# Kernel tuning notes

Measured on AMD Instinct MI355X. Metric: run time of the kernel, lower is better.

The kernel has to match this reference:

```python
import jax, jax.numpy as jnp
import numpy as np

T_KD = 20.0      # KL_divergence temperature
T_THR = 6.0      # Threshold_weights temperature
EPS = 1e-05


def _margin(o, gathered):
    # torch.sort descending, take top-2; margin only when target is the argmax value
    top2 = jax.lax.top_k(o, 2)[0]                      # [B, 2]
    return jnp.where(top2[:, 0] == gathered, top2[:, 0] - top2[:, 1], 0.0)


def _forward(outputs1, outputs2, outputs3, outputs4, out_s, targets):
    B = targets.shape[0]
    idx = jnp.arange(B)
    mimic = (outputs1 + outputs2 + outputs3 + outputs4) / 4.0

    teachers = [outputs1, outputs2, outputs3, outputs4, mimic]
    gathered = [t[idx, targets] for t in teachers]      # each [B]

    # C = min over gathered target logits of the 4 real teachers
    C = jnp.minimum(jnp.minimum(gathered[0].min(), gathered[1].min()),
                    jnp.minimum(gathered[2].min(), gathered[3].min()))
    # if C < 0: shift everything by (-C + eps); else no shift
    shift = jnp.where(C < 0, -C + EPS, 0.0)

    shifted = [t + shift for t in teachers]
    g_shift = [g + shift for g in gathered]

    # Threshold_weights: margin per branch, softmax over 5 branches
    preds = jnp.stack([_margin(s, g) for s, g in zip(shifted, g_shift)], axis=1)  # [B,5]
    out_threshold = jax.nn.softmax(preds / T_THR, axis=1)

    # max over the 4 (shifted) teacher logit tensors
    max_preds = jnp.maximum(jnp.maximum(shifted[0].max(), shifted[1].max()),
                            jnp.maximum(shifted[2].max(), shifted[3].max()))

    # per-sample CE of student (shared across branches)
    log_p_s = jax.nn.log_softmax(out_s, axis=1)
    CE = -log_p_s[idx, targets]                          # [B]

    log_ps_T = jax.nn.log_softmax(out_s / T_KD, axis=1)  # [B,C]

    def branch_loss(teacher, g_s):
        w2 = g_s / max_preds          # weights2
        w1 = 1.0 - w2                 # weights1
        log_pt = jax.nn.log_softmax(teacher / T_KD, axis=1)
        p_t = jnp.exp(log_pt)
        KD = jnp.sum(p_t * (log_pt - log_ps_T), axis=1) * (T_KD * T_KD)  # [B]
        return w1 * CE + w2 * KD

    # KD/CE use the ORIGINAL (unshifted) teacher logits
    losses = jnp.stack([branch_loss(t, g) for t, g in zip(teachers, g_shift)], axis=1)  # [B,5]
    return jnp.mean(jnp.sum(out_threshold * losses, axis=1))


def setup_inputs() -> dict:
    key = jax.random.key(0)
    ks = jax.random.split(key, 6)
    B, C = 8192, 1000
    return {
        "outputs1": jax.random.normal(ks[0], (B, C), dtype=jnp.float32),
        "outputs2": jax.random.normal(ks[1], (B, C), dtype=jnp.float32),
        "outputs3": jax.random.normal(ks[2], (B, C), dtype=jnp.float32),
        "outputs4": jax.random.normal(ks[3], (B, C), dtype=jnp.float32),
        "out_s": jax.random.normal(ks[4], (B, C), dtype=jnp.float32),
        "targets": jax.random.randint(ks[5], (B,), 0, C, dtype=jnp.int64 if jax.config.jax_enable_x64 else jnp.int32),
    }


def reference(outputs1, outputs2, outputs3, outputs4, out_s, targets):
    return _forward(outputs1, outputs2, outputs3, outputs4, out_s, targets)
```

## Files before the change

kernel.cpp:

```cpp
#include <hip/hip_runtime.h>
#include <math.h>

#define NB 8192
#define NC 1000
#define NF4 250


#define LOG2E 1.4426950408889634f
#define LN2   0.6931471805599453f
#define K20C  (LOG2E / 20.0f)

__device__ __forceinline__ float fexp2(float x) { return __builtin_amdgcn_exp2f(x); }
__device__ __forceinline__ float flog2(float x) { return __builtin_amdgcn_logf(x); }

#define VMWAIT0                                          \
  asm volatile("s_waitcnt vmcnt(0)" ::: "memory");       \
  __builtin_amdgcn_sched_barrier(0)
#define LGKM0                                            \
  asm volatile("s_waitcnt lgkmcnt(0)" ::: "memory");     \
  __builtin_amdgcn_sched_barrier(0)

typedef const __attribute__((address_space(1))) unsigned int gu32;
typedef __attribute__((address_space(3))) unsigned int lu32;
__device__ __forceinline__ void stage16(const void* g, void* l) {
  __builtin_amdgcn_global_load_lds((gu32*)g, (lu32*)l, 16, 0, 0);
}

template <int CTRL>
__device__ __forceinline__ float dpp_mov(float v, float ident) {
  return __uint_as_float((unsigned)__builtin_amdgcn_update_dpp(
      (int)__float_as_uint(ident), (int)__float_as_uint(v), CTRL, 0xF, 0xF,
      false));
}

__device__ __forceinline__ float dppredsum(float v) {
  v += dpp_mov<0x111>(v, 0.f);
  v += dpp_mov<0x112>(v, 0.f);
  v += dpp_mov<0x114>(v, 0.f);
  v += dpp_mov<0x118>(v, 0.f);
  v += dpp_mov<0x142>(v, 0.f);
  v += dpp_mov<0x143>(v, 0.f);
  return v;
}

__device__ __forceinline__ void dppredtop2(float& t1, float& t2) {
  const float NI = -INFINITY;
#define T2STEP(C)                                   \
  {                                                 \
    float i1 = dpp_mov<C>(t1, NI);                  \
    float i2 = dpp_mov<C>(t2, NI);                  \
    t2 = fmaxf(fmaxf(t2, i2), fminf(t1, i1));       \
    t1 = fmaxf(t1, i1);                             \
  }
  T2STEP(0x111) T2STEP(0x112) T2STEP(0x114) T2STEP(0x118)
  T2STEP(0x142) T2STEP(0x143)
#undef T2STEP
}

__device__ __forceinline__ float wredsum(float v) {
#pragma unroll
  for (int m = 32; m >= 1; m >>= 1) v += __shfl_xor(v, m, 64);
  return v;
}
__device__ __forceinline__ float wredmax(float v) {
#pragma unroll
  for (int m = 32; m >= 1; m >>= 1) v = fmaxf(v, __shfl_xor(v, m, 64));
  return v;
}
__device__ __forceinline__ float wredmin(float v) {
#pragma unroll
  for (int m = 32; m >= 1; m >>= 1) v = fminf(v, __shfl_xor(v, m, 64));
  return v;
}
__device__ __forceinline__ float f4get(const float4& v, int e) {
  return e == 0 ? v.x : e == 1 ? v.y : e == 2 ? v.z : v.w;
}
__device__ __forceinline__ float& f4ref(float4& v, int e) {
  return e == 0 ? v.x : e == 1 ? v.y : e == 2 ? v.z : v.w;
}

__device__ __forceinline__ void proc_mat(const float4& c, const float4& cs,
                                         float& t1, float& t2, float& Zm,
                                         float& S1m, float4& sum4) {
#pragma unroll
  for (int e = 0; e < 4; ++e) {
    float w = f4get(c, e);
    float wsv = f4get(cs, e);
    t2 = fmaxf(t2, fminf(t1, w));
    t1 = fmaxf(t1, w);
    float et = fexp2(w * K20C);
    Zm += et;
    S1m = fmaf(et, w - wsv, S1m);
    f4ref(sum4, e) += w;
  }
}

__global__ __launch_bounds__(256, 4) void k_rowstats(
    const float* __restrict__ o1, const float* __restrict__ o2,
    const float* __restrict__ o3, const float* __restrict__ o4,
    const float* __restrict__ os, const int* __restrict__ tg,
    float* __restrict__ ws, float* __restrict__ out) {
  const int lane = threadIdx.x & 63;
  const int wv = threadIdx.x >> 6;
  const int row = (blockIdx.x << 2) + wv;
  const size_t base = (size_t)row * NC;

  __shared__ float4 lds[4][5][64];

  if (blockIdx.x == 0 && threadIdx.x == 0) out[0] = 0.0f;

  const int target = tg[row];

#define STAGE(i)                                                          \
  do {                                                                    \
    int f_ = lane + ((i) << 6);                                           \
    if (f_ > NF4 - 1) f_ = NF4 - 1;    \
    stage16((const float4*)(o1 + base) + f_, &lds[wv][0][0]);             \
    stage16((const float4*)(o2 + base) + f_, &lds[wv][1][0]);             \
    stage16((const float4*)(o3 + base) + f_, &lds[wv][2][0]);             \
    stage16((const float4*)(o4 + base) + f_, &lds[wv][3][0]);             \
    stage16((const float4*)(os + base) + f_, &lds[wv][4][0]);             \
  } while (0)

  STAGE(0);

  float t1[5], t2[5], Z[5], S1[5];
#pragma unroll
  for (int t = 0; t < 5; ++t) {
    t1[t] = -INFINITY; t2[t] = -INFINITY; Z[t] = 0.f; S1[t] = 0.f;
  }
  float Z1 = 0.f, Z20 = 0.f;

#define CHUNK(ACT, STAGE_STMT)                                            \
  do {                                                                    \
    VMWAIT0;                                                              \
    float4 rs_ = lds[wv][4][lane];                                        \
    float4 sum4_ = {0.f, 0.f, 0.f, 0.f};                                  \
    float4 cm_;                                                           \
    cm_ = lds[wv][0][lane];                                               \
    if (ACT) proc_mat(cm_, rs_, t1[0], t2[0], Z[0], S1[0], sum4_);        \
    cm_ = lds[wv][1][lane];                                               \
    if (ACT) proc_mat(cm_, rs_, t1[1], t2[1], Z[1], S1[1], sum4_);        \
    cm_ = lds[wv][2][lane];                                               \
    if (ACT) proc_mat(cm_, rs_, t1[2], t2[2], Z[2], S1[2], sum4_);        \
    cm_ = lds[wv][3][lane];                                               \
    if (ACT) proc_mat(cm_, rs_, t1[3], t2[3], Z[3], S1[3], sum4_);        \
    LGKM0;     \
    STAGE_STMT;                                                           \
    if (ACT) {                                                            \
      _Pragma("unroll")                                                   \
      for (int e = 0; e < 4; ++e) {                                       \
        float wsv = f4get(rs_, e);                                        \
        float wm = f4get(sum4_, e) * 0.25f;                    \
        t2[4] = fmaxf(t2[4], fminf(t1[4], wm));                           \
        t1[4] = fmaxf(t1[4], wm);                                         \
        float et = fexp2(wm * K20C);                                      \
        Z[4] += et;                                                       \
        S1[4] = fmaf(et, wm - wsv, S1[4]);                                \
        Z1 += fexp2(wsv * LOG2E);                                         \
        Z20 += fexp2(wsv * K20C);                                         \
      }                                                                   \
    }                                                                     \
  } while (0)

  CHUNK(true, STAGE(1));
  CHUNK(true, STAGE(2));
  CHUNK(true, STAGE(3));
  CHUNK(lane < 58, );

  const float g1 = o1[base + target];
  const float g2 = o2[base + target];
  const float g3 = o3[base + target];
  const float g4 = o4[base + target];
  const float gs = os[base + target];

#pragma unroll
  for (int t = 0; t < 5; ++t) dppredtop2(t1[t], t2[t]);
#pragma unroll
  for (int t = 0; t < 5; ++t) { Z[t] = dppredsum(Z[t]); S1[t] = dppredsum(S1[t]); }
  Z1 = dppredsum(Z1);
  Z20 = dppredsum(Z20);

  if (lane == 63) {
    const float gm = ((g1 + g2) + g3 + g4) * 0.25f;
    float gg[5] = {g1, g2, g3, g4, gm};

    const float lse_s = flog2(Z20) * LN2;
    const float CE = flog2(Z1) * LN2 - gs;

#pragma unroll
    for (int t = 0; t < 5; ++t) {
      float lse_t = flog2(Z[t]) * LN2;
      float KD = 400.0f * (S1[t] / (20.0f * Z[t]) - lse_t + lse_s);
      float margin = (t1[t] == gg[t]) ? (t1[t] - t2[t]) : 0.0f;
      ws[(size_t)t * NB + row] = margin;
      ws[(size_t)(5 + t) * NB + row] = gg[t];
      ws[(size_t)(10 + t) * NB + row] = KD;
    }
    ws[(size_t)15 * NB + row] = CE;
    ws[(size_t)16 * NB + row] = fminf(fminf(g1, g2), fminf(g3, g4));
    ws[(size_t)17 * NB + row] = fmaxf(fmaxf(t1[0], t1[1]), fmaxf(t1[2], t1[3]));
  }
#undef STAGE
#undef CHUNK
}

__global__ __launch_bounds__(64) void k_final(const float* __restrict__ ws,
                                              float* __restrict__ out) {
  const int lane = threadIdx.x;

  float mn = INFINITY, mx = -INFINITY;
  const float4* mnp = (const float4*)(ws + (size_t)16 * NB);
  const float4* mxp = (const float4*)(ws + (size_t)17 * NB);
#pragma unroll
  for (int k = 0; k < 32; ++k) {
    int r4 = lane + (k << 6);
    float4 a = mnp[r4];
    float4 b = mxp[r4];
    mn = fminf(mn, fminf(fminf(a.x, a.y), fminf(a.z, a.w)));
    mx = fmaxf(mx, fmaxf(fmaxf(b.x, b.y), fmaxf(b.z, b.w)));
  }
  mn = wredmin(mn);
  mx = wredmax(mx);
  const float shift = (mn < 0.0f) ? (-mn + 1e-5f) : 0.0f;
  const float maxp = mx + shift;

  const int r = blockIdx.x * 64 + lane;
  const float K6 = LOG2E / 6.0f;

  float m[5], e[5];
#pragma unroll
  for (int t = 0; t < 5; ++t) m[t] = ws[(size_t)t * NB + r];
  float pm = fmaxf(fmaxf(fmaxf(m[0], m[1]), fmaxf(m[2], m[3])), m[4]);
  float Zl = 0.0f;
#pragma unroll
  for (int t = 0; t < 5; ++t) { e[t] = fexp2((m[t] - pm) * K6); Zl += e[t]; }
  float ce = ws[(size_t)15 * NB + r];
  float rl = 0.0f;
#pragma unroll
  for (int t = 0; t < 5; ++t) {
    float g = ws[(size_t)(5 + t) * NB + r];
    float kd = ws[(size_t)(10 + t) * NB + r];
    float w2 = (g + shift) / maxp;
    float loss = (1.0f - w2) * ce + w2 * kd;
    rl += e[t] * loss;
  }
  float acc = wredsum(rl / Zl);
  if (lane == 0) atomicAdd(out, acc * (1.0f / 8192.0f));
}

extern "C" void kernel_launch(void* const* d_in, const int* in_sizes, int n_in,
                              void* d_out, int out_size, void* d_ws, size_t ws_size,
                              hipStream_t stream) {
  const float* o1 = (const float*)d_in[0];
  const float* o2 = (const float*)d_in[1];
  const float* o3 = (const float*)d_in[2];
  const float* o4 = (const float*)d_in[3];
  const float* os = (const float*)d_in[4];
  const int* tg = (const int*)d_in[5];
  float* ws = (float*)d_ws;
  float* out = (float*)d_out;

  k_rowstats<<<NB / 4, 256, 0, stream>>>(o1, o2, o3, o4, os, tg, ws, out);
  k_final<<<NB / 64, 64, 0, stream>>>(ws, out);
}
```

Measured before the change: 187.4 us.

## Double-buffer LDS staging across four rows per wave with partial vmcnt waits

Each wave now processes four rows instead of one, using a two-slot LDS ring so the next chunk's global-to-LDS loads are in flight while the current chunk is computed. Partial s_waitcnt vmcnt counts replace full drains, and the target-logit gathers are issued early and overlapped with the streaming loads. The grid shrinks by four. The goal is to hide memory latency in this bandwidth-bound pass, at the cost of fewer blocks and fragile hand-counted wait values.

Result: no change. 189.9 us (+1.3%).

```diff
diff --git a/kernel.cpp b/kernel.cpp
--- a/kernel.cpp
+++ b/kernel.cpp
@@ -13,9 +13,10 @@
 __device__ __forceinline__ float fexp2(float x) { return __builtin_amdgcn_exp2f(x); }
 __device__ __forceinline__ float flog2(float x) { return __builtin_amdgcn_logf(x); }
 
-#define VMWAIT0                                          \
-  asm volatile("s_waitcnt vmcnt(0)" ::: "memory");       \
+#define VMWAIT_(N)                                       \
+  asm volatile("s_waitcnt vmcnt(" #N ")" ::: "memory");  \
   __builtin_amdgcn_sched_barrier(0)
+#define VMWAIT(N) VMWAIT_(N)
 #define LGKM0                                            \
   asm volatile("s_waitcnt lgkmcnt(0)" ::: "memory");     \
   __builtin_amdgcn_sched_barrier(0)
@@ -102,56 +103,98 @@
     float* __restrict__ ws, float* __restrict__ out) {
   const int lane = threadIdx.x & 63;
   const int wv = threadIdx.x >> 6;
-  const int row = (blockIdx.x << 2) + wv;
-  const size_t base = (size_t)row * NC;
-
-  __shared__ float4 lds[4][5][64];
+  const int rowbase = (blockIdx.x * 4 + wv) * 4;
+  __shared__ float4 lds[4][2][5][64];
 
   if (blockIdx.x == 0 && threadIdx.x == 0) out[0] = 0.0f;
 
-  const int target = tg[row];
-
-#define STAGE(i)                                                          \
-  do {                                                                    \
-    int f_ = lane + ((i) << 6);                                           \
+  int tgv = tg[rowbase + (lane & 3)];
+
+#define STAGES(s)                                                         \
+  do {                                                                    \
+    const int r_ = (s) >> 2, c_ = (s) & 3;                                \
+    const size_t b_ = (size_t)(rowbase + r_) * NC;                        \
+    int f_ = lane + (c_ << 6);                                            \
     if (f_ > NF4 - 1) f_ = NF4 - 1;    \
-    stage16((const float4*)(o1 + base) + f_, &lds[wv][0][0]);             \
-    stage16((const float4*)(o2 + base) + f_, &lds[wv][1][0]);             \
-    stage16((const float4*)(o3 + base) + f_, &lds[wv][2][0]);             \
-    stage16((const float4*)(o4 + base) + f_, &lds[wv][3][0]);             \
-    stage16((const float4*)(os + base) + f_, &lds[wv][4][0]);             \
-  } while (0)
-
-  STAGE(0);
-
-  float t1[5], t2[5], Z[5], S1[5];
-#pragma unroll
-  for (int t = 0; t < 5; ++t) {
-    t1[t] = -INFINITY; t2[t] = -INFINITY; Z[t] = 0.f; S1[t] = 0.f;
-  }
-  float Z1 = 0.f, Z20 = 0.f;
-
-#define CHUNK(ACT, STAGE_STMT)                                            \
-  do {                                                                    \
-    VMWAIT0;                                                              \
-    float4 rs_ = lds[wv][4][lane];                                        \
+    stage16((const float4*)(o1 + b_) + f_, &lds[wv][(s) & 1][0][0]);      \
+    stage16((const float4*)(o2 + b_) + f_, &lds[wv][(s) & 1][1][0]);      \
+    stage16((const float4*)(o3 + b_) + f_, &lds[wv][(s) & 1][2][0]);      \
+    stage16((const float4*)(o4 + b_) + f_, &lds[wv][(s) & 1][3][0]);      \
+    stage16((const float4*)(os + b_) + f_, &lds[wv][(s) & 1][4][0]);      \
+  } while (0)
+
+#define GATHER(r)                                                         \
+  do {                                                                    \
+    const int tgt_ = __shfl(tgv, (r), 64);                                \
+    const size_t gb_ = (size_t)(rowbase + (r)) * NC + tgt_;               \
+    g1 = o1[gb_]; g2 = o2[gb_]; g3 = o3[gb_]; g4 = o4[gb_]; g5 = os[gb_]; \
+  } while (0)
+
+  STAGES(0);
+  STAGES(1);
+
+  float t1[5], t2[5], Z[5], S1[5], Z1, Z20;
+  float g1, g2, g3, g4, g5;
+#define RESETACC                                                          \
+  do {                                                                    \
+    _Pragma("unroll") for (int t = 0; t < 5; ++t) {                       \
+      t1[t] = -INFINITY; t2[t] = -INFINITY; Z[t] = 0.f; S1[t] = 0.f;      \
+    }                                                                     \
+    Z1 = 0.f; Z20 = 0.f;                                                  \
+  } while (0)
+  RESETACC;
+
+#define REDUCE_EPI(r)                                                     \
+  do {                                                                    \
+    _Pragma("unroll") for (int t = 0; t < 5; ++t) dppredtop2(t1[t], t2[t]); \
+    _Pragma("unroll") for (int t = 0; t < 5; ++t) {                       \
+      Z[t] = dppredsum(Z[t]); S1[t] = dppredsum(S1[t]);                   \
+    }                                                                     \
+    Z1 = dppredsum(Z1);                                                   \
+    Z20 = dppredsum(Z20);                                                 \
+    if (lane == 63) {                                                     \
+      const int row_ = rowbase + (r);                                     \
+      const float gm_ = ((g1 + g2) + g3 + g4) * 0.25f;                    \
+      float gg_[5] = {g1, g2, g3, g4, gm_};                               \
+      const float lse_s_ = flog2(Z20) * LN2;                              \
+      const float CE_ = flog2(Z1) * LN2 - g5;                             \
+      _Pragma("unroll") for (int t = 0; t < 5; ++t) {                     \
+        float lse_t_ = flog2(Z[t]) * LN2;                                 \
+        float KD_ = 400.0f * (S1[t] / (20.0f * Z[t]) - lse_t_ + lse_s_);  \
+        float mg_ = (t1[t] == gg_[t]) ? (t1[t] - t2[t]) : 0.0f;           \
+        ws[(size_t)t * NB + row_] = mg_;                                  \
+        ws[(size_t)(5 + t) * NB + row_] = gg_[t];                         \
+        ws[(size_t)(10 + t) * NB + row_] = KD_;                           \
+      }                                                                   \
+      ws[(size_t)15 * NB + row_] = CE_;                                   \
+      ws[(size_t)16 * NB + row_] = fminf(fminf(g1, g2), fminf(g3, g4));   \
+      ws[(size_t)17 * NB + row_] =                                        \
+          fmaxf(fmaxf(t1[0], t1[1]), fmaxf(t1[2], t1[3]));                \
+    }                                                                     \
+    RESETACC;                                                             \
+  } while (0)
+
+#define SLOT(WAITN, BUF, ACT, STAGE_STMT, GATHER_STMT, ROWEND_STMT)       \
+  do {                                                                    \
+    VMWAIT(WAITN);                                                        \
+    float4 rs_ = lds[wv][BUF][4][lane];                                   \
     float4 sum4_ = {0.f, 0.f, 0.f, 0.f};                                  \
     float4 cm_;                                                           \
-    cm_ = lds[wv][0][lane];                                               \
+    cm_ = lds[wv][BUF][0][lane];                                          \
     if (ACT) proc_mat(cm_, rs_, t1[0], t2[0], Z[0], S1[0], sum4_);        \
-    cm_ = lds[wv][1][lane];                                               \
+    cm_ = lds[wv][BUF][1][lane];                                          \
     if (ACT) proc_mat(cm_, rs_, t1[1], t2[1], Z[1], S1[1], sum4_);        \
-    cm_ = lds[wv][2][lane];                                               \
+    cm_ = lds[wv][BUF][2][lane];                                          \
     if (ACT) proc_mat(cm_, rs_, t1[2], t2[2], Z[2], S1[2], sum4_);        \
-    cm_ = lds[wv][3][lane];                                               \
+    cm_ = lds[wv][BUF][3][lane];                                          \
     if (ACT) proc_mat(cm_, rs_, t1[3], t2[3], Z[3], S1[3], sum4_);        \
-    LGKM0;     \
+    LGKM0;              \
     STAGE_STMT;                                                           \
+    GATHER_STMT;                                                          \
     if (ACT) {                                                            \
-      _Pragma("unroll")                                                   \
-      for (int e = 0; e < 4; ++e) {                                       \
+      _Pragma("unroll") for (int e = 0; e < 4; ++e) {                     \
         float wsv = f4get(rs_, e);                                        \
-        float wm = f4get(sum4_, e) * 0.25f;                    \
+        float wm = f4get(sum4_, e) * 0.25f;                               \
         t2[4] = fmaxf(t2[4], fminf(t1[4], wm));                           \
         t1[4] = fmaxf(t1[4], wm);                                         \
         float et = fexp2(wm * K20C);                                      \
@@ -161,48 +204,31 @@
         Z20 += fexp2(wsv * K20C);                                         \
       }                                                                   \
     }                                                                     \
-  } while (0)
-
-  CHUNK(true, STAGE(1));
-  CHUNK(true, STAGE(2));
-  CHUNK(true, STAGE(3));
-  CHUNK(lane < 58, );
-
-  const float g1 = o1[base + target];
-  const float g2 = o2[base + target];
-  const float g3 = o3[base + target];
-  const float g4 = o4[base + target];
-  const float gs = os[base + target];
-
-#pragma unroll
-  for (int t = 0; t < 5; ++t) dppredtop2(t1[t], t2[t]);
-#pragma unroll
-  for (int t = 0; t < 5; ++t) { Z[t] = dppredsum(Z[t]); S1[t] = dppredsum(S1[t]); }
-  Z1 = dppredsum(Z1);
-  Z20 = dppredsum(Z20);
-
-  if (lane == 63) {
-    const float gm = ((g1 + g2) + g3 + g4) * 0.25f;
-    float gg[5] = {g1, g2, g3, g4, gm};
-
-    const float lse_s = flog2(Z20) * LN2;
-    const float CE = flog2(Z1) * LN2 - gs;
-
-#pragma unroll
-    for (int t = 0; t < 5; ++t) {
-      float lse_t = flog2(Z[t]) * LN2;
-      float KD = 400.0f * (S1[t] / (20.0f * Z[t]) - lse_t + lse_s);
-      float margin = (t1[t] == gg[t]) ? (t1[t] - t2[t]) : 0.0f;
-      ws[(size_t)t * NB + row] = margin;
-      ws[(size_t)(5 + t) * NB + row] = gg[t];
-      ws[(size_t)(10 + t) * NB + row] = KD;
-    }
-    ws[(size_t)15 * NB + row] = CE;
-    ws[(size_t)16 * NB + row] = fminf(fminf(g1, g2), fminf(g3, g4));
-    ws[(size_t)17 * NB + row] = fmaxf(fmaxf(t1[0], t1[1]), fmaxf(t1[2], t1[3]));
-  }
-#undef STAGE
-#undef CHUNK
+    ROWEND_STMT;                                                          \
+  } while (0)
+
+  SLOT(5,  0, true,      STAGES(2),  GATHER(0), );
+  SLOT(10, 1, true,      STAGES(3),  ,          );
+  SLOT(10, 0, true,      STAGES(4),  ,          );
+  SLOT(5,  1, lane < 58, STAGES(5),  ,          REDUCE_EPI(0));
+  SLOT(23, 0, true,      STAGES(6),  GATHER(1), );
+  SLOT(28, 1, true,      STAGES(7),  ,          );
+  SLOT(10, 0, true,      STAGES(8),  ,          );
+  SLOT(5,  1, lane < 58, STAGES(9),  ,          REDUCE_EPI(1));
+  SLOT(23, 0, true,      STAGES(10), GATHER(2), );
+  SLOT(28, 1, true,      STAGES(11), ,          );
+  SLOT(10, 0, true,      STAGES(12), ,          );
+  SLOT(5,  1, lane < 58, STAGES(13), ,          REDUCE_EPI(2));
+  SLOT(23, 0, true,      STAGES(14), GATHER(3), );
+  SLOT(28, 1, true,      STAGES(15), ,          );
+  SLOT(10, 0, true,      ,           ,          );
+  SLOT(0,  1, lane < 58, ,           ,          REDUCE_EPI(3));
+
+#undef STAGES
+#undef GATHER
+#undef RESETACC
+#undef REDUCE_EPI
+#undef SLOT
 }
 
 __global__ __launch_bounds__(64) void k_final(const float* __restrict__ ws,
@@ -261,6 +287,6 @@
   float* ws = (float*)d_ws;
   float* out = (float*)d_out;
 
-  k_rowstats<<<NB / 4, 256, 0, stream>>>(o1, o2, o3, o4, os, tg, ws, out);
+  k_rowstats<<<NB / 16, 256, 0, stream>>>(o1, o2, o3, o4, os, tg, ws, out);
   k_final<<<NB / 64, 64, 0, stream>>>(ws, out);
 }
```
